# Optimization experiments

Hardware: AMD Instinct MI355X
Metric: run time of the kernel (lower is better)

Reference implementation:

```python
import jax, jax.numpy as jnp
import numpy as np
from jax import lax

N_GAUSS = 32768
M_POINTS = 8192
BLOCK = 256
MAX_SCALE = 0.02
BG = -1.0


def setup_inputs() -> dict:
    key = jax.random.key(0)
    k = jax.random.split(key, 6)
    # query points in [-1, 1]^3 (forward maps them to [0,1]^3)
    x = jax.random.uniform(k[0], (M_POINTS, 3), jnp.float32) * 2.0 - 1.0
    xyz = jax.random.uniform(k[1], (N_GAUSS, 3), jnp.float32)          # means in [0,1]^3
    weight_raw = jax.random.normal(k[2], (N_GAUSS, 1), jnp.float32)
    scaling_raw = jax.random.normal(k[3], (N_GAUSS, 3), jnp.float32) * 0.3 + jnp.log(0.01)
    rotation_raw = jax.random.normal(k[4], (N_GAUSS, 4), jnp.float32)
    values_raw = jax.random.normal(k[5], (N_GAUSS, 1), jnp.float32)
    return {"x": x, "xyz": xyz, "weight_raw": weight_raw,
            "scaling_raw": scaling_raw, "rotation_raw": rotation_raw,
            "values_raw": values_raw}


def _quat_to_rotmat(q):
    # q: [N,4] normalized quaternion (w, x, y, z)
    w, x, y, z = q[:, 0], q[:, 1], q[:, 2], q[:, 3]
    r00 = 1 - 2 * (y * y + z * z); r01 = 2 * (x * y - w * z); r02 = 2 * (x * z + w * y)
    r10 = 2 * (x * y + w * z); r11 = 1 - 2 * (x * x + z * z); r12 = 2 * (y * z - w * x)
    r20 = 2 * (x * z - w * y); r21 = 2 * (y * z + w * x); r22 = 1 - 2 * (x * x + y * y)
    return jnp.stack([jnp.stack([r00, r01, r02], -1),
                      jnp.stack([r10, r11, r12], -1),
                      jnp.stack([r20, r21, r22], -1)], -2)  # [N,3,3]


def _splat(x, xyz, weight_raw, scaling_raw, rotation_raw, values_raw):
    p = (x + 1.0) / 2.0  # [M,3] in [0,1]^3
    # activations (match VEGS properties)
    s = jnp.exp(scaling_raw)                                  # [N,3]
    r = jnp.linalg.norm(s, axis=1, keepdims=True) + 1e-8
    r_soft = MAX_SCALE * jnp.tanh(r / MAX_SCALE)
    s = s * (r_soft / r)                                      # capped scales
    q = rotation_raw / (jnp.linalg.norm(rotation_raw, axis=1, keepdims=True) + 1e-12)
    R = _quat_to_rotmat(q)                                    # [N,3,3]
    inv_cov = jnp.einsum('nij,nj,nkj->nik', R, 1.0 / (s * s), R)  # Sigma^-1 = R S^-2 R^T
    w = jax.nn.sigmoid(weight_raw)[:, 0]                      # [N]
    v = jax.nn.sigmoid(values_raw)[:, 0]                      # [N]

    def block_fn(_, pb):
        # pb: [B,3]
        d = pb[:, None, :] - xyz[None, :, :]                  # [B,N,3]
        quad = jnp.einsum('bni,nij,bnj->bn', d, inv_cov, d)   # Mahalanobis^2
        alpha = w[None, :] * jnp.exp(-0.5 * quad)             # [B,N]
        num = alpha @ v                                       # [B]
        den = jnp.sum(alpha, axis=1)                          # [B]
        yb = jnp.where(den > 1e-8, num, BG)                   # empty cells -> bg = -1
        return None, yb

    nb = M_POINTS // BLOCK
    _, ys = lax.scan(block_fn, None, p.reshape(nb, BLOCK, 3))
    return ys.reshape(-1, 1)


def reference(x, xyz, weight_raw, scaling_raw, rotation_raw, values_raw):
    return _splat(x, xyz, weight_raw, scaling_raw, rotation_raw, values_raw)
```

## Files before the change

### kernel.cpp

```cpp
#include <hip/hip_runtime.h>

#define NG 32768
#define MP 8192
#define BG_VAL (-1.0f)
#define MAX_SCALE 0.02f

#define HALF_LOG2E 0.72134752044448170f
#define LOG2E      1.44269504088896340f

#define NC 4
#define NCELL 64
#define CELLW 0.25f
#define INV_CELLW 4.0f
#define RADF 7.899f

#define NSG 32
#define SCG 256
#define GCAP (NSG * SCG)
#define NSP 4
#define SCP 96
#define PCAP (NSP * SCP)

__device__ __forceinline__ float fast_rcp(float x)  { return __builtin_amdgcn_rcpf(x); }
__device__ __forceinline__ float fast_exp2(float x) { return __builtin_amdgcn_exp2f(x); }
__device__ __forceinline__ float fast_exp(float x)  { return fast_exp2(x * LOG2E); }
__device__ __forceinline__ float fast_sigmoid(float x) { return fast_rcp(1.0f + fast_exp(-x)); }

__global__ __launch_bounds__(256) void vegs_build(
    const float* __restrict__ xyz,
    const float* __restrict__ weight_raw,
    const float* __restrict__ scaling_raw,
    const float* __restrict__ rotation_raw,
    const float* __restrict__ values_raw,
    float4* __restrict__ gp,
    float4* __restrict__ gr)
{
    const int n = blockIdx.x * 256 + threadIdx.x;
    if (n >= NG) return;

    float s0 = fast_exp(scaling_raw[n * 3 + 0]);
    float s1 = fast_exp(scaling_raw[n * 3 + 1]);
    float s2 = fast_exp(scaling_raw[n * 3 + 2]);
    float r = sqrtf(s0 * s0 + s1 * s1 + s2 * s2) + 1e-8f;
    float y = r * (1.0f / MAX_SCALE);
    float E = fast_exp2(2.0f * LOG2E * y);
    float th = (E - 1.0f) * fast_rcp(E + 1.0f);
    float k = (MAX_SCALE * th) * fast_rcp(r);
    s0 *= k; s1 *= k; s2 *= k;

    float i0 = fast_rcp(s0 * s0);
    float i1 = fast_rcp(s1 * s1);
    float i2 = fast_rcp(s2 * s2);

    float qw = rotation_raw[n * 4 + 0];
    float qx = rotation_raw[n * 4 + 1];
    float qy = rotation_raw[n * 4 + 2];
    float qz = rotation_raw[n * 4 + 3];
    float qn = sqrtf(qw * qw + qx * qx + qy * qy + qz * qz) + 1e-12f;
    float iq = fast_rcp(qn);
    qw *= iq; qx *= iq; qy *= iq; qz *= iq;

    float r00 = 1.0f - 2.0f * (qy * qy + qz * qz);
    float r01 = 2.0f * (qx * qy - qw * qz);
    float r02 = 2.0f * (qx * qz + qw * qy);
    float r10 = 2.0f * (qx * qy + qw * qz);
    float r11 = 1.0f - 2.0f * (qx * qx + qz * qz);
    float r12 = 2.0f * (qy * qz - qw * qx);
    float r20 = 2.0f * (qx * qz - qw * qy);
    float r21 = 2.0f * (qy * qz + qw * qx);
    float r22 = 1.0f - 2.0f * (qx * qx + qy * qy);

    float G00 = r00 * r00 * i0 + r01 * r01 * i1 + r02 * r02 * i2;
    float G11 = r10 * r10 * i0 + r11 * r11 * i1 + r12 * r12 * i2;
    float G22 = r20 * r20 * i0 + r21 * r21 * i1 + r22 * r22 * i2;
    float G01 = r00 * r10 * i0 + r01 * r11 * i1 + r02 * r12 * i2;
    float G02 = r00 * r20 * i0 + r01 * r21 * i1 + r02 * r22 * i2;
    float G12 = r10 * r20 * i0 + r11 * r21 * i1 + r12 * r22 * i2;

    float w  = fast_sigmoid(weight_raw[n]);
    float v  = fast_sigmoid(values_raw[n]);
    float m0 = xyz[n * 3 + 0];
    float m1 = xyz[n * 3 + 1];
    float m2 = xyz[n * 3 + 2];

    const float c = HALF_LOG2E;
    float h0 = 2.0f * c * (G00 * m0 + G01 * m1 + G02 * m2);
    float h1 = 2.0f * c * (G01 * m0 + G11 * m1 + G12 * m2);
    float h2 = 2.0f * c * (G02 * m0 + G12 * m1 + G22 * m2);
    float k0 = -0.5f * (h0 * m0 + h1 * m1 + h2 * m2);

    gp[n * 3 + 0] = make_float4(-c * G00, -c * G11, -c * G22, -2.0f * c * G01);
    gp[n * 3 + 1] = make_float4(-2.0f * c * G02, -2.0f * c * G12, h0, h1);
    gp[n * 3 + 2] = make_float4(h2, k0, w, w * v);

    float smax = fmaxf(s0, fmaxf(s1, s2));
    gr[n] = make_float4(m0, m1, m2, RADF * smax);
}

__global__ __launch_bounds__(64) void vegs_bin(
    const float* __restrict__ x,
    const float4* __restrict__ gr,
    const float4* __restrict__ gp,
    float4* __restrict__ cslab,
    float4* __restrict__ spt,
    int* __restrict__ gcount,
    int* __restrict__ pcount)
{
    const int bid  = blockIdx.x;
    const int lane = threadIdx.x;

    if (bid < NCELL * NSG) {
        const int c = bid / NSG;
        const int s = bid - c * NSG;
        const int cx = c & 3, cy = (c >> 2) & 3, cz = c >> 4;
        const float lo0 = cx * CELLW, hi0 = lo0 + CELLW;
        const float lo1 = cy * CELLW, hi1 = lo1 + CELLW;
        const float lo2 = cz * CELLW, hi2 = lo2 + CELLW;
        float4* __restrict__ slab = cslab + ((size_t)c * GCAP + s * SCG) * 3;

        const int beg = s * (NG / NSG);
        const int end = beg + (NG / NSG);
        int cnt = 0;
        #pragma unroll 4
        for (int base = beg; base < end; base += 64) {
            const int gid = base + lane;
            float4 g = gr[gid];
            float dx = fmaxf(fmaxf(lo0 - g.x, g.x - hi0), 0.0f);
            float dy = fmaxf(fmaxf(lo1 - g.y, g.y - hi1), 0.0f);
            float dz = fmaxf(fmaxf(lo2 - g.z, g.z - hi2), 0.0f);
            bool hit = (dx * dx + dy * dy + dz * dz) <= g.w * g.w;
            unsigned long long mask = __ballot(hit);
            int pos = cnt + __popcll(mask & ((1ULL << lane) - 1ULL));
            if (hit && pos < SCG) {
                slab[pos * 3 + 0] = gp[gid * 3 + 0];
                slab[pos * 3 + 1] = gp[gid * 3 + 1];
                slab[pos * 3 + 2] = gp[gid * 3 + 2];
            }
            cnt += __popcll(mask);
        }
        if (lane == 0) gcount[bid] = min(cnt, SCG);
    } else {
        const int pb = bid - NCELL * NSG;
        const int c = pb / NSP;
        const int s = pb - c * NSP;
        float4* __restrict__ slab = spt + (size_t)c * PCAP + s * SCP;

        const int beg = s * (MP / NSP);
        const int end = beg + (MP / NSP);
        int cnt = 0;
        #pragma unroll 4
        for (int base = beg; base < end; base += 64) {
            const int m = base + lane;
            float p0 = (x[m * 3 + 0] + 1.0f) * 0.5f;
            float p1 = (x[m * 3 + 1] + 1.0f) * 0.5f;
            float p2 = (x[m * 3 + 2] + 1.0f) * 0.5f;
            int cx = min(NC - 1, max(0, (int)(p0 * INV_CELLW)));
            int cy = min(NC - 1, max(0, (int)(p1 * INV_CELLW)));
            int cz = min(NC - 1, max(0, (int)(p2 * INV_CELLW)));
            bool hit = (cx + NC * (cy + NC * cz)) == c;
            unsigned long long mask = __ballot(hit);
            int pos = cnt + __popcll(mask & ((1ULL << lane) - 1ULL));
            if (hit && pos < SCP)
                slab[pos] = make_float4(p0, p1, p2, __int_as_float(m));
            cnt += __popcll(mask);
        }
        if (lane == 0) pcount[pb] = min(cnt, SCP);
    }
}

__global__ __launch_bounds__(64) void vegs_cellmain(
    const float4* __restrict__ cslab,
    const float4* __restrict__ spt,
    const int* __restrict__ gcount,
    const int* __restrict__ pcount,
    float2* __restrict__ partial)
{
    const int c    = blockIdx.x;
    const int pb   = blockIdx.y;
    const int k    = blockIdx.z;
    const int lane = threadIdx.x;

    const int n0 = pcount[c * NSP + 0];
    const int n1 = pcount[c * NSP + 1];
    const int n2 = pcount[c * NSP + 2];
    const int n3 = pcount[c * NSP + 3];
    const int c1 = n0, c2 = c1 + n1, c3 = c2 + n2;
    const int nt = c3 + n3;
    if (pb * 128 >= nt) return;

    const int  piA  = pb * 128 + lane;
    const int  piB  = piA + 64;
    const bool actA = piA < nt;
    const bool actB = piB < nt;
    const int  peA  = actA ? piA : 0;
    const int  peB  = actB ? piB : 0;

    int sA = (peA >= c1) + (peA >= c2) + (peA >= c3);
    int cumA = (sA == 0) ? 0 : ((sA == 1) ? c1 : ((sA == 2) ? c2 : c3));
    int sB = (peB >= c1) + (peB >= c2) + (peB >= c3);
    int cumB = (sB == 0) ? 0 : ((sB == 1) ? c1 : ((sB == 2) ? c2 : c3));

    float4 PA = spt[c * PCAP + sA * SCP + (peA - cumA)];
    float4 PB = spt[c * PCAP + sB * SCP + (peB - cumB)];
    const float a0 = PA.x, a1 = PA.y, a2 = PA.z;
    const float b0 = PB.x, b1 = PB.y, b2 = PB.z;

    const float4* __restrict__ base = cslab + ((size_t)c * GCAP + k * SCG) * 3;
    const int glen = gcount[c * NSG + k];

    float numA = 0.0f, denA = 0.0f;
    float numB = 0.0f, denB = 0.0f;

    #pragma unroll 4
    for (int j = 0; j < glen; ++j) {
        float4 A0 = base[j * 3 + 0];
        float4 A1 = base[j * 3 + 1];
        float4 A2 = base[j * 3 + 2];

        float t0 = fmaf(A0.x, a0, A1.z);
        t0 = fmaf(A0.w, a1, t0);
        t0 = fmaf(A1.x, a2, t0);
        float t1 = fmaf(A0.y, a1, A1.w);
        t1 = fmaf(A1.y, a2, t1);
        float t2 = fmaf(A0.z, a2, A2.x);
        float qA = fmaf(a0, t0, A2.y);
        qA = fmaf(a1, t1, qA);
        qA = fmaf(a2, t2, qA);
        float eA = fast_exp2(qA);
        denA = fmaf(A2.z, eA, denA);
        numA = fmaf(A2.w, eA, numA);

        float u0 = fmaf(A0.x, b0, A1.z);
        u0 = fmaf(A0.w, b1, u0);
        u0 = fmaf(A1.x, b2, u0);
        float u1 = fmaf(A0.y, b1, A1.w);
        u1 = fmaf(A1.y, b2, u1);
        float u2 = fmaf(A0.z, b2, A2.x);
        float qB = fmaf(b0, u0, A2.y);
        qB = fmaf(b1, u1, qB);
        qB = fmaf(b2, u2, qB);
        float eB = fast_exp2(qB);
        denB = fmaf(A2.z, eB, denB);
        numB = fmaf(A2.w, eB, numB);
    }

    if (actA) partial[(size_t)k * (NCELL * PCAP) + c * PCAP + piA] = make_float2(numA, denA);
    if (actB) partial[(size_t)k * (NCELL * PCAP) + c * PCAP + piB] = make_float2(numB, denB);
}

__global__ __launch_bounds__(256) void vegs_reduce(
    const float2* __restrict__ partial,
    const float4* __restrict__ spt,
    const int* __restrict__ pcount,
    float* __restrict__ out)
{
    const int g  = blockIdx.x * 256 + threadIdx.x;
    const int c  = g / PCAP;
    const int pi = g - c * PCAP;

    const int n0 = pcount[c * NSP + 0];
    const int n1 = pcount[c * NSP + 1];
    const int n2 = pcount[c * NSP + 2];
    const int n3 = pcount[c * NSP + 3];
    const int c1 = n0, c2 = c1 + n1, c3 = c2 + n2;
    const int nt = c3 + n3;
    if (pi >= nt) return;

    float num = 0.0f, den = 0.0f;
    #pragma unroll 8
    for (int k = 0; k < NSG; ++k) {
        float2 p = partial[(size_t)k * (NCELL * PCAP) + g];
        num += p.x;
        den += p.y;
    }

    int s = (pi >= c1) + (pi >= c2) + (pi >= c3);
    int cum = (s == 0) ? 0 : ((s == 1) ? c1 : ((s == 2) ? c2 : c3));
    int orig = __float_as_int(spt[c * PCAP + s * SCP + (pi - cum)].w);
    out[orig] = (den > 1e-8f) ? num : BG_VAL;
}

extern "C" void kernel_launch(void* const* d_in, const int* in_sizes, int n_in,
                              void* d_out, int out_size, void* d_ws, size_t ws_size,
                              hipStream_t stream) {
    const float* x            = (const float*)d_in[0];
    const float* xyz          = (const float*)d_in[1];
    const float* weight_raw   = (const float*)d_in[2];
    const float* scaling_raw  = (const float*)d_in[3];
    const float* rotation_raw = (const float*)d_in[4];
    const float* values_raw   = (const float*)d_in[5];
    float* out = (float*)d_out;

    char* ws = (char*)d_ws;
    size_t off = 0;
    float4* gp    = (float4*)(ws + off); off += (size_t)NG * 3 * sizeof(float4);
    float4* gr    = (float4*)(ws + off); off += (size_t)NG * sizeof(float4);
    float4* spt   = (float4*)(ws + off); off += (size_t)NCELL * PCAP * sizeof(float4);
    float4* cslab = (float4*)(ws + off); off += (size_t)NCELL * GCAP * 3 * sizeof(float4);
    float2* partial = (float2*)(ws + off); off += (size_t)NSG * NCELL * PCAP * sizeof(float2);
    int* gcount = (int*)(ws + off); off += (size_t)NCELL * NSG * sizeof(int);
    int* pcount = (int*)(ws + off); off += (size_t)NCELL * NSP * sizeof(int);

    vegs_build<<<NG / 256, 256, 0, stream>>>(
        xyz, weight_raw, scaling_raw, rotation_raw, values_raw, gp, gr);

    vegs_bin<<<NCELL * NSG + NCELL * NSP, 64, 0, stream>>>(
        x, gr, gp, cslab, spt, gcount, pcount);

    dim3 mg(NCELL, PCAP / 128, NSG);
    vegs_cellmain<<<mg, 64, 0, stream>>>(cslab, spt, gcount, pcount, partial);

    vegs_reduce<<<NCELL * PCAP / 256, 256, 0, stream>>>(partial, spt, pcount, out);
}
```

Baseline: 104.1 us.

## Fuse Gaussian parameter build into binning kernel, recomputing per cell

Removes the separate build kernel and its gp/gr intermediate buffers. Each binning block now reads the raw scales and means, computes the capped radius for the cell test, and evaluates the full inverse covariance only for Gaussians that hit the cell. This saves one launch and the global round-trip of the precomputed parameters. In exchange, the scale activation is recomputed 64 times per Gaussian (once per cell) and the unroll drops from 4 to 2.

```diff
diff --git a/kernel.cpp b/kernel.cpp
--- a/kernel.cpp
+++ b/kernel.cpp
@@ -21,86 +21,21 @@
 #define SCP 96
 #define PCAP (NSP * SCP)
 
+#define GJOBS (NCELL * NSG)
+#define PJOBS (NCELL * NSP)
+
 __device__ __forceinline__ float fast_rcp(float x)  { return __builtin_amdgcn_rcpf(x); }
 __device__ __forceinline__ float fast_exp2(float x) { return __builtin_amdgcn_exp2f(x); }
 __device__ __forceinline__ float fast_exp(float x)  { return fast_exp2(x * LOG2E); }
 __device__ __forceinline__ float fast_sigmoid(float x) { return fast_rcp(1.0f + fast_exp(-x)); }
 
-__global__ __launch_bounds__(256) void vegs_build(
+__global__ __launch_bounds__(64) void vegs_bin(
+    const float* __restrict__ x,
     const float* __restrict__ xyz,
     const float* __restrict__ weight_raw,
     const float* __restrict__ scaling_raw,
     const float* __restrict__ rotation_raw,
     const float* __restrict__ values_raw,
-    float4* __restrict__ gp,
-    float4* __restrict__ gr)
-{
-    const int n = blockIdx.x * 256 + threadIdx.x;
-    if (n >= NG) return;
-
-    float s0 = fast_exp(scaling_raw[n * 3 + 0]);
-    float s1 = fast_exp(scaling_raw[n * 3 + 1]);
-    float s2 = fast_exp(scaling_raw[n * 3 + 2]);
-    float r = sqrtf(s0 * s0 + s1 * s1 + s2 * s2) + 1e-8f;
-    float y = r * (1.0f / MAX_SCALE);
-    float E = fast_exp2(2.0f * LOG2E * y);
-    float th = (E - 1.0f) * fast_rcp(E + 1.0f);
-    float k = (MAX_SCALE * th) * fast_rcp(r);
-    s0 *= k; s1 *= k; s2 *= k;
-
-    float i0 = fast_rcp(s0 * s0);
-    float i1 = fast_rcp(s1 * s1);
-    float i2 = fast_rcp(s2 * s2);
-
-    float qw = rotation_raw[n * 4 + 0];
-    float qx = rotation_raw[n * 4 + 1];
-    float qy = rotation_raw[n * 4 + 2];
-    float qz = rotation_raw[n * 4 + 3];
-    float qn = sqrtf(qw * qw + qx * qx + qy * qy + qz * qz) + 1e-12f;
-    float iq = fast_rcp(qn);
-    qw *= iq; qx *= iq; qy *= iq; qz *= iq;
-
-    float r00 = 1.0f - 2.0f * (qy * qy + qz * qz);
-    float r01 = 2.0f * (qx * qy - qw * qz);
-    float r02 = 2.0f * (qx * qz + qw * qy);
-    float r10 = 2.0f * (qx * qy + qw * qz);
-    float r11 = 1.0f - 2.0f * (qx * qx + qz * qz);
-    float r12 = 2.0f * (qy * qz - qw * qx);
-    float r20 = 2.0f * (qx * qz - qw * qy);
-    float r21 = 2.0f * (qy * qz + qw * qx);
-    float r22 = 1.0f - 2.0f * (qx * qx + qy * qy);
-
-    float G00 = r00 * r00 * i0 + r01 * r01 * i1 + r02 * r02 * i2;
-    float G11 = r10 * r10 * i0 + r11 * r11 * i1 + r12 * r12 * i2;
-    float G22 = r20 * r20 * i0 + r21 * r21 * i1 + r22 * r22 * i2;
-    float G01 = r00 * r10 * i0 + r01 * r11 * i1 + r02 * r12 * i2;
-    float G02 = r00 * r20 * i0 + r01 * r21 * i1 + r02 * r22 * i2;
-    float G12 = r10 * r20 * i0 + r11 * r21 * i1 + r12 * r22 * i2;
-
-    float w  = fast_sigmoid(weight_raw[n]);
-    float v  = fast_sigmoid(values_raw[n]);
-    float m0 = xyz[n * 3 + 0];
-    float m1 = xyz[n * 3 + 1];
-    float m2 = xyz[n * 3 + 2];
-
-    const float c = HALF_LOG2E;
-    float h0 = 2.0f * c * (G00 * m0 + G01 * m1 + G02 * m2);
-    float h1 = 2.0f * c * (G01 * m0 + G11 * m1 + G12 * m2);
-    float h2 = 2.0f * c * (G02 * m0 + G12 * m1 + G22 * m2);
-    float k0 = -0.5f * (h0 * m0 + h1 * m1 + h2 * m2);
-
-    gp[n * 3 + 0] = make_float4(-c * G00, -c * G11, -c * G22, -2.0f * c * G01);
-    gp[n * 3 + 1] = make_float4(-2.0f * c * G02, -2.0f * c * G12, h0, h1);
-    gp[n * 3 + 2] = make_float4(h2, k0, w, w * v);
-
-    float smax = fmaxf(s0, fmaxf(s1, s2));
-    gr[n] = make_float4(m0, m1, m2, RADF * smax);
-}
-
-__global__ __launch_bounds__(64) void vegs_bin(
-    const float* __restrict__ x,
-    const float4* __restrict__ gr,
-    const float4* __restrict__ gp,
     float4* __restrict__ cslab,
     float4* __restrict__ spt,
     int* __restrict__ gcount,
@@ -109,7 +44,7 @@
     const int bid  = blockIdx.x;
     const int lane = threadIdx.x;
 
-    if (bid < NCELL * NSG) {
+    if (bid < GJOBS) {
         const int c = bid / NSG;
         const int s = bid - c * NSG;
         const int cx = c & 3, cy = (c >> 2) & 3, cz = c >> 4;
@@ -121,26 +56,81 @@
         const int beg = s * (NG / NSG);
         const int end = beg + (NG / NSG);
         int cnt = 0;
-        #pragma unroll 4
+        #pragma unroll 2
         for (int base = beg; base < end; base += 64) {
-            const int gid = base + lane;
-            float4 g = gr[gid];
-            float dx = fmaxf(fmaxf(lo0 - g.x, g.x - hi0), 0.0f);
-            float dy = fmaxf(fmaxf(lo1 - g.y, g.y - hi1), 0.0f);
-            float dz = fmaxf(fmaxf(lo2 - g.z, g.z - hi2), 0.0f);
-            bool hit = (dx * dx + dy * dy + dz * dz) <= g.w * g.w;
+            const int n = base + lane;
+
+            float s0 = fast_exp(scaling_raw[n * 3 + 0]);
+            float s1 = fast_exp(scaling_raw[n * 3 + 1]);
+            float s2 = fast_exp(scaling_raw[n * 3 + 2]);
+            float r = sqrtf(s0 * s0 + s1 * s1 + s2 * s2) + 1e-8f;
+            float y = r * (1.0f / MAX_SCALE);
+            float E = fast_exp2(2.0f * LOG2E * y);
+            float th = (E - 1.0f) * fast_rcp(E + 1.0f);
+            float kk = (MAX_SCALE * th) * fast_rcp(r);
+            s0 *= kk; s1 *= kk; s2 *= kk;
+
+            float m0 = xyz[n * 3 + 0];
+            float m1 = xyz[n * 3 + 1];
+            float m2 = xyz[n * 3 + 2];
+
+            float R = RADF * fmaxf(s0, fmaxf(s1, s2));
+            float dx = fmaxf(fmaxf(lo0 - m0, m0 - hi0), 0.0f);
+            float dy = fmaxf(fmaxf(lo1 - m1, m1 - hi1), 0.0f);
+            float dz = fmaxf(fmaxf(lo2 - m2, m2 - hi2), 0.0f);
+            bool hit = (dx * dx + dy * dy + dz * dz) <= R * R;
+
             unsigned long long mask = __ballot(hit);
             int pos = cnt + __popcll(mask & ((1ULL << lane) - 1ULL));
+
             if (hit && pos < SCG) {
-                slab[pos * 3 + 0] = gp[gid * 3 + 0];
-                slab[pos * 3 + 1] = gp[gid * 3 + 1];
-                slab[pos * 3 + 2] = gp[gid * 3 + 2];
+                float i0 = fast_rcp(s0 * s0);
+                float i1 = fast_rcp(s1 * s1);
+                float i2 = fast_rcp(s2 * s2);
+
+                float qw = rotation_raw[n * 4 + 0];
+                float qx = rotation_raw[n * 4 + 1];
+                float qy = rotation_raw[n * 4 + 2];
+                float qz = rotation_raw[n * 4 + 3];
+                float qn = sqrtf(qw * qw + qx * qx + qy * qy + qz * qz) + 1e-12f;
+                float iq = fast_rcp(qn);
+                qw *= iq; qx *= iq; qy *= iq; qz *= iq;
+
+                float r00 = 1.0f - 2.0f * (qy * qy + qz * qz);
+                float r01 = 2.0f * (qx * qy - qw * qz);
+                float r02 = 2.0f * (qx * qz + qw * qy);
+                float r10 = 2.0f * (qx * qy + qw * qz);
+                float r11 = 1.0f - 2.0f * (qx * qx + qz * qz);
+                float r12 = 2.0f * (qy * qz - qw * qx);
+                float r20 = 2.0f * (qx * qz - qw * qy);
+                float r21 = 2.0f * (qy * qz + qw * qx);
+                float r22 = 1.0f - 2.0f * (qx * qx + qy * qy);
+
+                float G00 = r00 * r00 * i0 + r01 * r01 * i1 + r02 * r02 * i2;
+                float G11 = r10 * r10 * i0 + r11 * r11 * i1 + r12 * r12 * i2;
+                float G22 = r20 * r20 * i0 + r21 * r21 * i1 + r22 * r22 * i2;
+                float G01 = r00 * r10 * i0 + r01 * r11 * i1 + r02 * r12 * i2;
+                float G02 = r00 * r20 * i0 + r01 * r21 * i1 + r02 * r22 * i2;
+                float G12 = r10 * r20 * i0 + r11 * r21 * i1 + r12 * r22 * i2;
+
+                float w  = fast_sigmoid(weight_raw[n]);
+                float v  = fast_sigmoid(values_raw[n]);
+
+                const float cc = HALF_LOG2E;
+                float h0 = 2.0f * cc * (G00 * m0 + G01 * m1 + G02 * m2);
+                float h1 = 2.0f * cc * (G01 * m0 + G11 * m1 + G12 * m2);
+                float h2 = 2.0f * cc * (G02 * m0 + G12 * m1 + G22 * m2);
+                float k0 = -0.5f * (h0 * m0 + h1 * m1 + h2 * m2);
+
+                slab[pos * 3 + 0] = make_float4(-cc * G00, -cc * G11, -cc * G22, -2.0f * cc * G01);
+                slab[pos * 3 + 1] = make_float4(-2.0f * cc * G02, -2.0f * cc * G12, h0, h1);
+                slab[pos * 3 + 2] = make_float4(h2, k0, w, w * v);
             }
             cnt += __popcll(mask);
         }
         if (lane == 0) gcount[bid] = min(cnt, SCG);
     } else {
-        const int pb = bid - NCELL * NSG;
+        const int pb = bid - GJOBS;
         const int c = pb / NSP;
         const int s = pb - c * NSP;
         float4* __restrict__ slab = spt + (size_t)c * PCAP + s * SCP;
@@ -293,19 +283,15 @@
 
     char* ws = (char*)d_ws;
     size_t off = 0;
-    float4* gp    = (float4*)(ws + off); off += (size_t)NG * 3 * sizeof(float4);
-    float4* gr    = (float4*)(ws + off); off += (size_t)NG * sizeof(float4);
     float4* spt   = (float4*)(ws + off); off += (size_t)NCELL * PCAP * sizeof(float4);
     float4* cslab = (float4*)(ws + off); off += (size_t)NCELL * GCAP * 3 * sizeof(float4);
     float2* partial = (float2*)(ws + off); off += (size_t)NSG * NCELL * PCAP * sizeof(float2);
     int* gcount = (int*)(ws + off); off += (size_t)NCELL * NSG * sizeof(int);
     int* pcount = (int*)(ws + off); off += (size_t)NCELL * NSP * sizeof(int);
 
-    vegs_build<<<NG / 256, 256, 0, stream>>>(
-        xyz, weight_raw, scaling_raw, rotation_raw, values_raw, gp, gr);
-
-    vegs_bin<<<NCELL * NSG + NCELL * NSP, 64, 0, stream>>>(
-        x, gr, gp, cslab, spt, gcount, pcount);
+    vegs_bin<<<GJOBS + PJOBS, 64, 0, stream>>>(
+        x, xyz, weight_raw, scaling_raw, rotation_raw, values_raw,
+        cslab, spt, gcount, pcount);
 
     dim3 mg(NCELL, PCAP / 128, NSG);
     vegs_cellmain<<<mg, 64, 0, stream>>>(cslab, spt, gcount, pcount, partial);
```

New measurement: 104.7 us. No clear change (+0.5%).
